# Performance work log

Measured on AMD Instinct MI355X. Metric: run time of the kernel, lower is better.

Reference implementation:

```python
import jax, jax.numpy as jnp
import numpy as np

CODEBOOK_SIZE = 8192
EMBED_DIM = 128
BETA = 0.25
TEMPERATURE = 0.1
EPS_NORM = 1e-12  # torch F.normalize eps


def _l2_normalize(x, axis=-1):
    n = jnp.linalg.norm(x, axis=axis, keepdims=True)
    return x / jnp.maximum(n, EPS_NORM)


def setup_inputs() -> dict:
    key = jax.random.key(0)
    kz, kw = jax.random.split(key)
    z = jax.random.normal(kz, (4, 4096, EMBED_DIM), dtype=jnp.float32)
    # torch init is uniform(-1/D, 1/D); normal also exercises the math fine,
    # but stay faithful to scale:
    W = jax.random.uniform(kw, (CODEBOOK_SIZE, EMBED_DIM), dtype=jnp.float32,
                           minval=-1.0 / EMBED_DIM, maxval=1.0 / EMBED_DIM)
    return {"z": z, "W": W}


def reference(z, W):
    orig_shape = z.shape
    z_flat = z.reshape(-1, EMBED_DIM)              # [N, D]
    N = z_flat.shape[0]

    z_norm = _l2_normalize(z_flat, axis=1)
    e_norm = _l2_normalize(W, axis=1)
    scores = z_norm @ e_norm.T                     # [N, K]

    idx = jnp.argmax(scores, axis=1)               # [N]
    z_q = W[idx].reshape(orig_shape)

    counts = jnp.zeros((CODEBOOK_SIZE,), jnp.float32).at[idx].add(1.0)
    e_mean = counts / N
    perplexity = jnp.exp(-jnp.sum(e_mean * jnp.log(e_mean + 1e-8)))

    sg = jax.lax.stop_gradient
    commit_loss = jnp.mean((sg(z_q) - z) ** 2) + BETA * jnp.mean((z_q - sg(z)) ** 2)

    z_q_st = z + sg(z_q - z)                        # straight-through

    log_probs = jax.nn.log_softmax(scores / TEMPERATURE, axis=1)  # [N, K]
    probs = jnp.exp(log_probs)
    P_avg = jnp.mean(probs, axis=0) + 1e-8
    entropy_loss = -jnp.sum(P_avg * jnp.log(P_avg))

    return (z_q_st, commit_loss, perplexity, entropy_loss)
```

## Files before the change

### kernel.cpp

```cpp
#include <hip/hip_runtime.h>
#include <hip/hip_bf16.h>
#include <math.h>

#define N_ROWS 16384
#define DIM 128
#define K_CODES 8192
#define SCALE_LOG2E 14.4269504088896341f
#define EPS2 0.0288539f
#define EPSF 1.00989e-3f

#define OFF_EN       0u
#define OFF_ZN       1048576u
#define OFF_EP       3145728u
#define OFF_ZP       4194304u
#define OFF_ZC       6291456u
#define OFF_PART     7340032u
#define OFF_PART2    7602176u
#define OFF_LINV     7864320u
#define OFF_IDX      7880704u
#define OFF_FLA      7897088u
#define OFF_FLB      7913472u
#define OFF_CNT      7929856u
#define OFF_P        7938048u
#define OFF_MSE      7946240u
#define OFF_NFA      7946241u
#define OFF_NFB      7946242u
#define OFF_REFBUF   7946244u
#define MEMSET_BYTES 196624u

typedef __bf16 bf16x8 __attribute__((ext_vector_type(8)));
typedef float  f32x4  __attribute__((ext_vector_type(4)));
#define MFMA16(a, b, c) __builtin_amdgcn_mfma_f32_16x16x32_bf16(a, b, c, 0, 0, 0)

#if defined(__has_builtin)
#if __has_builtin(__builtin_amdgcn_exp2f)
#define EXP2(x) __builtin_amdgcn_exp2f(x)
#endif
#endif
#ifndef EXP2
#define EXP2(x) __expf(0.69314718055994531f * (x))
#endif

__device__ __forceinline__ void gld_lds16(const ushort* g, ushort* l) {
    __builtin_amdgcn_global_load_lds(
        (const __attribute__((address_space(1))) unsigned int*)g,
        (__attribute__((address_space(3))) unsigned int*)l, 16, 0, 0);
}

__device__ __forceinline__ ushort f2bf(float x) {
    __hip_bfloat16 b = __float2bfloat16(x);
    return *reinterpret_cast<ushort*>(&b);
}
__device__ __forceinline__ float bf2f(ushort u) {
    __hip_bfloat16 b = *reinterpret_cast<__hip_bfloat16*>(&u);
    return __bfloat162float(b);
}

__device__ __forceinline__ void bf_store2(ushort* __restrict__ P, int T, int r,
                                          int rx, int k, ushort e0, ushort e1) {
    int g = k >> 6, kp = (k >> 3) & 7, j = k & 7;
    int off = (((((T << 2) + g) << 10) + (r << 3) + (kp ^ rx)) << 3) + j;
    *reinterpret_cast<ushort2*>(&P[off]) = make_ushort2(e0, e1);
}

__global__ __launch_bounds__(256) void k_prep(const float* __restrict__ z,
                                              const float* __restrict__ W,
                                              float* __restrict__ zN,
                                              float* __restrict__ eN,
                                              ushort* __restrict__ Zp,
                                              ushort* __restrict__ Ep) {
    int t = threadIdx.x, w = t >> 6, lane = t & 63;
    int row = blockIdx.x * 4 + w;
    const float* src; float* dstN; ushort* dstP; float sc;
    if (row < N_ROWS) { src = z; dstN = zN; dstP = Zp; sc = SCALE_LOG2E; }
    else { row -= N_ROWS; src = W; dstN = eN; dstP = Ep; sc = 1.0f; }
    float2 v = *reinterpret_cast<const float2*>(&src[(size_t)row * DIM + lane * 2]);
    float ss = v.x * v.x + v.y * v.y;
#pragma unroll
    for (int off = 32; off; off >>= 1) ss += __shfl_xor(ss, off);
    float nrm = fmaxf(sqrtf(ss), 1e-12f);
    float a = v.x / nrm, b = v.y / nrm;
    *reinterpret_cast<float2*>(&dstN[(size_t)row * DIM + lane * 2]) = make_float2(a, b);
    float as = a * sc, bs = b * sc;
    ushort ha = f2bf(as), hb = f2bf(bs);
    ushort la = f2bf(as - bf2f(ha)), lb = f2bf(bs - bf2f(hb));
    int T = row >> 7, r = row & 127, rx = r & 7, d = lane * 2;
    bf_store2(dstP, T, r, rx, d, ha, hb);
    bf_store2(dstP, T, r, rx, 128 + d, la, lb);
}

__global__ __launch_bounds__(256, 4) void k_p1(const ushort* __restrict__ Zp,
                                               const ushort* __restrict__ Ep,
                                               float4* __restrict__ part) {
    __shared__ ushort Bu[2][8192];
    int t = threadIdx.x, lane = t & 63, w = t >> 6;
    int rg = blockIdx.x >> 2, slice = blockIdx.x & 3;
    int wm = w >> 1, wn = w & 1;
    int n15 = lane & 15, quad = lane >> 4;
    int T = rg >> 1, rofs = (rg & 1) << 6;

    bf16x8 af[2][2][2];
#pragma unroll
    for (int ms = 0; ms < 2; ++ms) {
        int r = rofs + wm * 32 + ms * 16 + n15, rx = r & 7;
#pragma unroll
        for (int g = 0; g < 2; ++g)
#pragma unroll
            for (int kl = 0; kl < 2; ++kl)
                af[ms][g][kl] = *reinterpret_cast<const bf16x8*>(
                    &Zp[(((((T << 2) + g) << 10) + (r << 3) + (((kl * 4 + quad)) ^ rx)) << 3)]);
    }

    float sm[8], s2v[8], sl[8];
    unsigned si[8];
#pragma unroll
    for (int s = 0; s < 8; ++s) { sm[s] = -1e30f; s2v[s] = -1e30f; sl[s] = 0.f; si[s] = 0u; }

    {
        int Te = slice * 16, re = 0;
#pragma unroll
        for (int it = 0; it < 4; ++it) {
            int cpos = it * 256 + t;
            int g = cpos >> 9, loc = cpos & 511;
            gld_lds16(Ep + ((((Te << 2) + g) << 13) + (re << 6) + (loc << 3)),
                      &Bu[0][cpos << 3]);
        }
    }
    int bufc = 0;
    for (int ch = 0; ch < 32; ++ch) {
        __syncthreads();
        if (ch < 31) {
            int nx = ch + 1;
            int Te = slice * 16 + (nx >> 1), re = (nx & 1) << 6;
            ushort* dst = Bu[bufc ^ 1];
#pragma unroll
            for (int it = 0; it < 4; ++it) {
                int cpos = it * 256 + t;
                int g = cpos >> 9, loc = cpos & 511;
                gld_lds16(Ep + ((((Te << 2) + g) << 13) + (re << 6) + (loc << 3)),
                          &dst[cpos << 3]);
            }
        }
        const ushort* bsrc = Bu[bufc];
        f32x4 acc[2][2];
#pragma unroll
        for (int i = 0; i < 2; ++i)
#pragma unroll
            for (int j = 0; j < 2; ++j) acc[i][j] = (f32x4)2.0f;
#pragma unroll
        for (int g = 0; g < 2; ++g)
#pragma unroll
            for (int kl = 0; kl < 2; ++kl) {
                bf16x8 bfr[2];
#pragma unroll
                for (int ns = 0; ns < 2; ++ns) {
                    int c = wn * 32 + ns * 16 + n15;
                    int kx = (kl * 4 + quad) ^ (c & 7);
                    bfr[ns] = *reinterpret_cast<const bf16x8*>(
                        &bsrc[(((g << 9) + (c << 3) + kx) << 3)]);
                }
#pragma unroll
                for (int ms = 0; ms < 2; ++ms)
#pragma unroll
                    for (int ns = 0; ns < 2; ++ns)
                        acc[ms][ns] = MFMA16(af[ms][g][kl], bfr[ns], acc[ms][ns]);
            }
        unsigned cbase = (unsigned)(slice * 2048 + ch * 64 + wn * 32 + n15);
#pragma unroll
        for (int ms = 0; ms < 2; ++ms)
#pragma unroll
            for (int reg = 0; reg < 4; ++reg) {
                int s = ms * 4 + reg;
                float m = sm[s], m2 = s2v[s], l = sl[s];
                unsigned idx = si[s];
#pragma unroll
                for (int ns = 0; ns < 2; ++ns) {
                    float v = acc[ms][ns][reg];
                    l += EXP2(v);
                    m2 = __builtin_amdgcn_fmed3f(v, m, m2);
                    idx = (v > m) ? (cbase + ns * 16) : idx;
                    m = fmaxf(v, m);
                }
                sl[s] = l; sm[s] = m; s2v[s] = m2; si[s] = idx;
            }
        bufc ^= 1;
    }
#pragma unroll
    for (int ms = 0; ms < 2; ++ms)
#pragma unroll
        for (int reg = 0; reg < 4; ++reg) {
            int s = ms * 4 + reg;
            float m = sm[s], m2 = s2v[s], l = sl[s];
            unsigned idx = si[s];
#pragma unroll
            for (int off = 1; off < 16; off <<= 1) {
                float om  = __shfl_xor(m, off);
                float om2 = __shfl_xor(m2, off);
                float ol  = __shfl_xor(l, off);
                unsigned oi = (unsigned)__shfl_xor((int)idx, off);
                m2 = fmaxf(fmaxf(m2, om2), fminf(m, om));
                l += ol;
                bool take = (om > m) || (om == m && oi < idx);
                idx = take ? oi : idx;
                m = fmaxf(m, om);
            }
            if (n15 == 0) {
                int row = rg * 64 + wm * 32 + ms * 16 + quad * 4 + reg;
                part[slice * N_ROWS + row] = make_float4(m, l, __uint_as_float(idx), m2);
            }
        }
}

__global__ __launch_bounds__(256) void k_merge(const float4* __restrict__ part,
                                               float* __restrict__ linv_out,
                                               int* __restrict__ idx_out,
                                               unsigned int* __restrict__ counts,
                                               int* __restrict__ flaglistA,
                                               int* __restrict__ nfA) {
    int row = blockIdx.x * 256 + threadIdx.x;
    float m = -1e30f, m2 = -1e30f, l = 0.f;
    unsigned idx = 0u;
#pragma unroll
    for (int s = 0; s < 4; ++s) {
        float4 p = part[s * N_ROWS + row];
        float om = p.x, ol = p.y, om2 = p.w;
        unsigned oi = __float_as_uint(p.z);
        m2 = fmaxf(fmaxf(m2, om2), fminf(m, om));
        l += ol;
        bool take = (om > m) || (om == m && oi < idx);
        idx = take ? oi : idx;
        m = fmaxf(m, om);
    }
    linv_out[row] = 1.0f / l;
    idx_out[row] = (int)idx;
    atomicAdd(&counts[idx], 1u);
    if (m - m2 < EPS2) {
        int pos = atomicAdd(nfA, 1);
        if (pos < 8192) flaglistA[pos] = row;
    }
}

__global__ __launch_bounds__(256) void k_gather2(const ushort* __restrict__ Zp,
                                                 const int* __restrict__ flaglistA,
                                                 const int* __restrict__ nfA,
                                                 ushort* __restrict__ Zc) {
    int nf2 = *nfA; if (nf2 > 8192) nf2 = 8192;
    int total = nf2 * 32;
    const uint4* srcv = reinterpret_cast<const uint4*>(Zp);
    uint4* dstv = reinterpret_cast<uint4*>(Zc);
    for (int c = blockIdx.x * 256 + threadIdx.x; c < total; c += 65536) {
        int crow = c >> 5, g = (c >> 3) & 3, kp = c & 7;
        int row = flaglistA[crow];
        int Ts = row >> 7, rs = row & 127;
        int sidx = (((Ts << 2) + g) << 10) + (rs << 3) + (kp ^ (rs & 7));
        int Td = crow >> 6, rd = crow & 63;
        int didx = (((Td << 2) + g) << 9) + (rd << 3) + (kp ^ (rd & 7));
        dstv[didx] = srcv[sidx];
    }
}

__global__ __launch_bounds__(256, 2) void k_s2(const ushort* __restrict__ Zc,
                                               const ushort* __restrict__ Ep,
                                               const int* __restrict__ nfA,
                                               float4* __restrict__ part2) {
    __shared__ ushort Bu[2][8192];
    int nf2 = *nfA; if (nf2 > 8192) nf2 = 8192;
    int cg2 = blockIdx.x >> 3, csl = blockIdx.x & 7;
    if (cg2 * 64 >= nf2) return;
    int t = threadIdx.x, lane = t & 63, w = t >> 6;
    int wm = w >> 1, wn = w & 1;
    int n15 = lane & 15, quad = lane >> 4;

    bf16x8 af[2][4][2];
#pragma unroll
    for (int ms = 0; ms < 2; ++ms) {
        int r = wm * 32 + ms * 16 + n15, rx = r & 7;
#pragma unroll
        for (int gz = 0; gz < 4; ++gz)
#pragma unroll
            for (int kl = 0; kl < 2; ++kl)
                af[ms][gz][kl] = *reinterpret_cast<const bf16x8*>(
                    &Zc[(((((cg2 << 2) + gz) << 9) + (r << 3) + ((kl * 4 + quad) ^ rx)) << 3)]);
    }

    float sm[8], s2v[8];
    unsigned si[8];
#pragma unroll
    for (int s = 0; s < 8; ++s) { sm[s] = -1e30f; s2v[s] = -1e30f; si[s] = 0u; }

    {
        const ushort* gb = Ep + (((size_t)((csl * 8) << 2)) << 13);
#pragma unroll
        for (int it = 0; it < 4; ++it) {
            int cpos = it * 256 + t;
            gld_lds16(gb + (cpos << 3), &Bu[0][cpos << 3]);
        }
    }
    int bufc = 0;
    f32x4 acc[2][4];
#pragma unroll
    for (int i = 0; i < 2; ++i)
#pragma unroll
        for (int j = 0; j < 4; ++j) acc[i][j] = (f32x4)2.0f;

    for (int st = 0; st < 32; ++st) {
        __syncthreads();
        if (st < 31) {
            int nx = st + 1;
            const ushort* gb = Ep + (((size_t)(((csl * 8 + (nx >> 2)) << 2) + (nx & 3))) << 13);
            ushort* dst = Bu[bufc ^ 1];
#pragma unroll
            for (int it = 0; it < 4; ++it) {
                int cpos = it * 256 + t;
                gld_lds16(gb + (cpos << 3), &dst[cpos << 3]);
            }
        }
        const ushort* bsrc = Bu[bufc];
        int ge = st & 3;
        int a0 = ge & 1, a1 = (ge & 1) + 2;
        bool two = (ge < 2);
#pragma unroll
        for (int kl = 0; kl < 2; ++kl) {
            bf16x8 bfr[4];
#pragma unroll
            for (int ns = 0; ns < 4; ++ns) {
                int c = wn * 64 + ns * 16 + n15;
                int kx = (kl * 4 + quad) ^ (c & 7);
                bfr[ns] = *reinterpret_cast<const bf16x8*>(&bsrc[(((c << 3) + kx) << 3)]);
            }
#pragma unroll
            for (int ms = 0; ms < 2; ++ms)
#pragma unroll
                for (int ns = 0; ns < 4; ++ns)
                    acc[ms][ns] = MFMA16(af[ms][a0][kl], bfr[ns], acc[ms][ns]);
            if (two) {
#pragma unroll
                for (int ms = 0; ms < 2; ++ms)
#pragma unroll
                    for (int ns = 0; ns < 4; ++ns)
                        acc[ms][ns] = MFMA16(af[ms][a1][kl], bfr[ns], acc[ms][ns]);
            }
        }
        if (ge == 3) {
            int ch = st >> 2;
            unsigned cbase = (unsigned)((csl * 8 + ch) * 128 + wn * 64 + n15);
#pragma unroll
            for (int ms = 0; ms < 2; ++ms)
#pragma unroll
                for (int reg = 0; reg < 4; ++reg) {
                    int s = ms * 4 + reg;
                    float m = sm[s], m2 = s2v[s];
                    unsigned idx = si[s];
#pragma unroll
                    for (int ns = 0; ns < 4; ++ns) {
                        float v = acc[ms][ns][reg];
                        m2 = __builtin_amdgcn_fmed3f(v, m, m2);
                        idx = (v > m) ? (cbase + ns * 16) : idx;
                        m = fmaxf(v, m);
                    }
                    sm[s] = m; s2v[s] = m2; si[s] = idx;
                }
#pragma unroll
            for (int i = 0; i < 2; ++i)
#pragma unroll
                for (int j = 0; j < 4; ++j) acc[i][j] = (f32x4)2.0f;
        }
        bufc ^= 1;
    }
#pragma unroll
    for (int ms = 0; ms < 2; ++ms)
#pragma unroll
        for (int reg = 0; reg < 4; ++reg) {
            int s = ms * 4 + reg;
            float m = sm[s], m2 = s2v[s];
            unsigned idx = si[s];
#pragma unroll
            for (int off = 1; off < 16; off <<= 1) {
                float om  = __shfl_xor(m, off);
                float om2 = __shfl_xor(m2, off);
                unsigned oi = (unsigned)__shfl_xor((int)idx, off);
                m2 = fmaxf(fmaxf(m2, om2), fminf(m, om));
                bool take = (om > m) || (om == m && oi < idx);
                idx = take ? oi : idx;
                m = fmaxf(m, om);
            }
            if (n15 == 0) {
                int crow = cg2 * 64 + wm * 32 + ms * 16 + quad * 4 + reg;
                part2[csl * 8192 + crow] = make_float4(m, 0.f, __uint_as_float(idx), m2);
            }
        }
}

__global__ __launch_bounds__(256) void k_merge2(const float4* __restrict__ part2,
                                                const int* __restrict__ flaglistA,
                                                const int* __restrict__ nfA,
                                                int* __restrict__ idx_arr,
                                                unsigned int* __restrict__ counts,
                                                int* __restrict__ flaglistB,
                                                int* __restrict__ nfB) {
    int i = blockIdx.x * 256 + threadIdx.x;
    int nf2 = *nfA; if (nf2 > 8192) nf2 = 8192;
    if (i >= nf2) return;
    int row = flaglistA[i];
    float m = -1e30f, m2 = -1e30f;
    unsigned idx = 0u;
#pragma unroll
    for (int s = 0; s < 8; ++s) {
        float4 p = part2[s * 8192 + i];
        float om = p.x, om2 = p.w;
        unsigned oi = __float_as_uint(p.z);
        m2 = fmaxf(fmaxf(m2, om2), fminf(m, om));
        bool take = (om > m) || (om == m && oi < idx);
        idx = take ? oi : idx;
        m = fmaxf(m, om);
    }
    int newi = (int)idx, oldi = idx_arr[row];
    if (newi != oldi) {
        idx_arr[row] = newi;
        atomicAdd(&counts[oldi], 0xFFFFFFFFu);
        atomicAdd(&counts[newi], 1u);
    }
    if (m - m2 < EPSF) {
        int pos = atomicAdd(nfB, 1);
        if (pos < N_ROWS) flaglistB[pos] = row;
    }
}

__global__ __launch_bounds__(256) void k_refine(const float* __restrict__ zN,
                                                const float* __restrict__ eN,
                                                const int* __restrict__ flaglistB,
                                                const int* __restrict__ nfB,
                                                unsigned long long* __restrict__ refbuf) {
    int nf = *nfB;
    if (nf > N_ROWS) nf = N_ROWS;
    int csl = blockIdx.x & 7;
    int t = threadIdx.x;
    __shared__ float zl[DIM];
    for (int fi = blockIdx.x >> 3; fi < nf; fi += 512) {
        int row = flaglistB[fi];
        __syncthreads();
        if (t < DIM) zl[t] = zN[(size_t)row * DIM + t];
        __syncthreads();
        double best = -1e300;
        int bc = 0x7FFFFFFF;
#pragma unroll
        for (int j = 0; j < 4; ++j) {
            int c = csl * 1024 + j * 256 + t;
            const float* e = &eN[(size_t)c * DIM];
            double s = 0.0;
#pragma unroll 8
            for (int d = 0; d < DIM; ++d) s += (double)zl[d] * (double)e[d];
            if (s > best) { best = s; bc = c; }
        }
#pragma unroll
        for (int off = 1; off < 64; off <<= 1) {
            double ob = __shfl_xor(best, off);
            int oc = __shfl_xor(bc, off);
            if (ob > best || (ob == best && oc < bc)) { best = ob; bc = oc; }
        }
        if ((t & 63) == 0) {
            unsigned long long u = (unsigned long long)__double_as_longlong(best);
            u = (u & 0x8000000000000000ull) ? ~u : (u | 0x8000000000000000ull);
            unsigned long long key = (u & ~0x1FFFull) | (unsigned long long)(8191 - bc);
            atomicMax(&refbuf[row], key);
        }
    }
}

__global__ __launch_bounds__(256) void k_fixidx(const int* __restrict__ flaglistB,
                                                const int* __restrict__ nfB,
                                                const unsigned long long* __restrict__ refbuf,
                                                int* __restrict__ idx,
                                                unsigned int* __restrict__ counts) {
    int i = blockIdx.x * 256 + threadIdx.x;
    int nf = *nfB;
    if (nf > N_ROWS) nf = N_ROWS;
    if (i < nf) {
        int row = flaglistB[i];
        int newi = 8191 - (int)(refbuf[row] & 0x1FFFull);
        int oldi = idx[row];
        if (newi != oldi) {
            idx[row] = newi;
            atomicAdd(&counts[oldi], 0xFFFFFFFFu);
            atomicAdd(&counts[newi], 1u);
        }
    }
}

__global__ __launch_bounds__(256, 4) void k_p2(const ushort* __restrict__ Zp,
                                               const ushort* __restrict__ Ep,
                                               const float* __restrict__ linv_in,
                                               float* __restrict__ P_sum) {
    __shared__ ushort Bu[2][8192];
    int t = threadIdx.x, lane = t & 63, w = t >> 6;
    int cg = blockIdx.x >> 2, rslice = blockIdx.x & 3;
    int wm = w >> 1, wn = w & 1;
    int n15 = lane & 15, quad = lane >> 4;
    int T = cg >> 1, cofs = (cg & 1) << 6;

    bf16x8 af[2][2][2];
#pragma unroll
    for (int ms = 0; ms < 2; ++ms) {
        int c = cofs + wm * 32 + ms * 16 + n15, cx = c & 7;
#pragma unroll
        for (int g = 0; g < 2; ++g)
#pragma unroll
            for (int kl = 0; kl < 2; ++kl)
                af[ms][g][kl] = *reinterpret_cast<const bf16x8*>(
                    &Ep[(((((T << 2) + g) << 10) + (c << 3) + ((kl * 4 + quad) ^ cx)) << 3)]);
    }

    float pacc[8];
#pragma unroll
    for (int s = 0; s < 8; ++s) pacc[s] = 0.f;

    {
        int Tz = rslice * 32, re = 0;
#pragma unroll
        for (int it = 0; it < 4; ++it) {
            int cpos = it * 256 + t;
            int g = cpos >> 9, loc = cpos & 511;
            gld_lds16(Zp + ((((Tz << 2) + g) << 13) + (re << 6) + (loc << 3)),
                      &Bu[0][cpos << 3]);
        }
    }
    int bufc = 0;
    for (int ch = 0; ch < 64; ++ch) {
        __syncthreads();
        if (ch < 63) {
            int nx = ch + 1;
            int Tz = rslice * 32 + (nx >> 1), re = (nx & 1) << 6;
            ushort* dst = Bu[bufc ^ 1];
#pragma unroll
            for (int it = 0; it < 4; ++it) {
                int cpos = it * 256 + t;
                int g = cpos >> 9, loc = cpos & 511;
                gld_lds16(Zp + ((((Tz << 2) + g) << 13) + (re << 6) + (loc << 3)),
                          &dst[cpos << 3]);
            }
        }
        const ushort* bsrc = Bu[bufc];
        f32x4 acc[2][2];
#pragma unroll
        for (int i = 0; i < 2; ++i)
#pragma unroll
            for (int j = 0; j < 2; ++j) acc[i][j] = (f32x4)2.0f;
#pragma unroll
        for (int g = 0; g < 2; ++g)
#pragma unroll
            for (int kl = 0; kl < 2; ++kl) {
                bf16x8 bfr[2];
#pragma unroll
                for (int ns = 0; ns < 2; ++ns) {
                    int r = wn * 32 + ns * 16 + n15;
                    int kx = (kl * 4 + quad) ^ (r & 7);
                    bfr[ns] = *reinterpret_cast<const bf16x8*>(
                        &bsrc[(((g << 9) + (r << 3) + kx) << 3)]);
                }
#pragma unroll
                for (int ms = 0; ms < 2; ++ms)
#pragma unroll
                    for (int ns = 0; ns < 2; ++ns)
                        acc[ms][ns] = MFMA16(af[ms][g][kl], bfr[ns], acc[ms][ns]);
            }
        int rbase = rslice * 4096 + ch * 64 + wn * 32 + n15;
        float li[2];
#pragma unroll
        for (int ns = 0; ns < 2; ++ns) li[ns] = linv_in[rbase + ns * 16];
#pragma unroll
        for (int ms = 0; ms < 2; ++ms)
#pragma unroll
            for (int reg = 0; reg < 4; ++reg) {
                int s = ms * 4 + reg;
                float p = pacc[s];
#pragma unroll
                for (int ns = 0; ns < 2; ++ns)
                    p = fmaf(EXP2(acc[ms][ns][reg]), li[ns], p);
                pacc[s] = p;
            }
        bufc ^= 1;
    }
#pragma unroll
    for (int s = 0; s < 8; ++s) {
#pragma unroll
        for (int off = 1; off < 16; off <<= 1) pacc[s] += __shfl_xor(pacc[s], off);
    }
    if (n15 == 0) {
#pragma unroll
        for (int ms = 0; ms < 2; ++ms)
#pragma unroll
            for (int reg = 0; reg < 4; ++reg)
                atomicAdd(&P_sum[cg * 64 + wm * 32 + ms * 16 + quad * 4 + reg],
                          pacc[ms * 4 + reg]);
    }
}

__global__ __launch_bounds__(256) void k_gather(const float* __restrict__ z,
                                                const float* __restrict__ W,
                                                const int* __restrict__ idx,
                                                float* __restrict__ out,
                                                float* __restrict__ mse) {
    int v = blockIdx.x * 256 + threadIdx.x;
    int row = v >> 5;
    int id = idx[row];
    float4 q = *reinterpret_cast<const float4*>(&W[(size_t)id * DIM + (v & 31) * 4]);
    float4 zz = *reinterpret_cast<const float4*>(&z[(size_t)v * 4]);
    float dx = q.x - zz.x, dy = q.y - zz.y, dz = q.z - zz.z, dw = q.w - zz.w;
    *reinterpret_cast<float4*>(&out[(size_t)v * 4]) = q;
    float e = dx * dx + dy * dy + dz * dz + dw * dw;
#pragma unroll
    for (int off = 1; off < 64; off <<= 1) e += __shfl_xor(e, off);
    __shared__ float red[4];
    int lane = threadIdx.x & 63, wv = threadIdx.x >> 6;
    if (lane == 0) red[wv] = e;
    __syncthreads();
    if (threadIdx.x == 0) atomicAdd(mse, red[0] + red[1] + red[2] + red[3]);
}

__global__ __launch_bounds__(256) void k_finalize(const unsigned int* __restrict__ counts,
                                                  const float* __restrict__ P_sum,
                                                  const float* __restrict__ mse,
                                                  float* __restrict__ out) {
    int t = threadIdx.x;
    float s1 = 0.f, s2 = 0.f;
    for (int k = t; k < K_CODES; k += 256) {
        float em = (float)counts[k] * (1.0f / 16384.0f);
        s1 += em * logf(em + 1e-8f);
        float p = P_sum[k] * (1.0f / 16384.0f) + 1e-8f;
        s2 += p * logf(p);
    }
#pragma unroll
    for (int off = 1; off < 64; off <<= 1) {
        s1 += __shfl_xor(s1, off);
        s2 += __shfl_xor(s2, off);
    }
    __shared__ float r1[4], r2[4];
    int lane = t & 63, wv = t >> 6;
    if (lane == 0) { r1[wv] = s1; r2[wv] = s2; }
    __syncthreads();
    if (t == 0) {
        float S1 = r1[0] + r1[1] + r1[2] + r1[3];
        float S2 = r2[0] + r2[1] + r2[2] + r2[3];
        out[2097152] = 1.25f * mse[0] * (1.0f / 2097152.0f);
        out[2097153] = expf(-S1);
        out[2097154] = -S2;
    }
}

extern "C" void kernel_launch(void* const* d_in, const int* in_sizes, int n_in,
                              void* d_out, int out_size, void* d_ws, size_t ws_size,
                              hipStream_t stream) {
    (void)in_sizes; (void)n_in; (void)out_size; (void)ws_size;
    const float* z = (const float*)d_in[0];
    const float* W = (const float*)d_in[1];
    float* ws = (float*)d_ws;
    float* eN = ws + OFF_EN;
    float* zN = ws + OFF_ZN;
    ushort* Ep = (ushort*)(ws + OFF_EP);
    ushort* Zp = (ushort*)(ws + OFF_ZP);
    ushort* Zc = (ushort*)(ws + OFF_ZC);
    float4* part = (float4*)(ws + OFF_PART);
    float4* part2 = (float4*)(ws + OFF_PART2);
    float* linv = ws + OFF_LINV;
    int* idx = (int*)(ws + OFF_IDX);
    int* flaglistA = (int*)(ws + OFF_FLA);
    int* flaglistB = (int*)(ws + OFF_FLB);
    unsigned int* counts = (unsigned int*)(ws + OFF_CNT);
    float* P = ws + OFF_P;
    float* mse = ws + OFF_MSE;
    int* nfA = (int*)(ws + OFF_NFA);
    int* nfB = (int*)(ws + OFF_NFB);
    unsigned long long* refbuf = (unsigned long long*)(ws + OFF_REFBUF);
    float* out = (float*)d_out;

    hipMemsetAsync(ws + OFF_CNT, 0, MEMSET_BYTES, stream);
    k_prep<<<(N_ROWS + K_CODES) / 4, 256, 0, stream>>>(z, W, zN, eN, Zp, Ep);
    k_p1<<<1024, 256, 0, stream>>>(Zp, Ep, part);
    k_merge<<<N_ROWS / 256, 256, 0, stream>>>(part, linv, idx, counts, flaglistA, nfA);
    k_gather2<<<256, 256, 0, stream>>>(Zp, flaglistA, nfA, Zc);
    k_s2<<<1024, 256, 0, stream>>>(Zc, Ep, nfA, part2);
    k_merge2<<<32, 256, 0, stream>>>(part2, flaglistA, nfA, idx, counts, flaglistB, nfB);
    k_refine<<<4096, 256, 0, stream>>>(zN, eN, flaglistB, nfB, refbuf);
    k_fixidx<<<64, 256, 0, stream>>>(flaglistB, nfB, refbuf, idx, counts);
    k_p2<<<512, 256, 0, stream>>>(Zp, Ep, linv, P);
    k_gather<<<(N_ROWS * DIM / 4) / 256, 256, 0, stream>>>(z, W, idx, out, mse);
    k_finalize<<<1, 256, 0, stream>>>(counts, P, mse, out);
}
```

Measured before the change: 299.0 us.

## Drop intermediate bf16 rescoring stage and spread MSE atomics across slots

Removes the gather2/s2/merge2 second-pass bf16 rescoring of ambiguous rows, so every row flagged by the first merge goes straight to the fp32 exact refine kernel. This cuts three kernel launches and a partial GEMM. In exchange, refine may process more rows, since the flag list is no longer narrowed by the tighter EPSF threshold. The MSE reduction now writes to 256 padded partial slots instead of a single atomic, and finalize reduces those slots.

```diff
diff --git a/kernel.cpp b/kernel.cpp
--- a/kernel.cpp
+++ b/kernel.cpp
@@ -7,26 +7,23 @@
 #define K_CODES 8192
 #define SCALE_LOG2E 14.4269504088896341f
 #define EPS2 0.0288539f
-#define EPSF 1.00989e-3f
 
 #define OFF_EN       0u
 #define OFF_ZN       1048576u
 #define OFF_EP       3145728u
 #define OFF_ZP       4194304u
-#define OFF_ZC       6291456u
 #define OFF_PART     7340032u
-#define OFF_PART2    7602176u
 #define OFF_LINV     7864320u
 #define OFF_IDX      7880704u
 #define OFF_FLA      7897088u
-#define OFF_FLB      7913472u
 #define OFF_CNT      7929856u
 #define OFF_P        7938048u
 #define OFF_MSE      7946240u
 #define OFF_NFA      7946241u
 #define OFF_NFB      7946242u
 #define OFF_REFBUF   7946244u
-#define MEMSET_BYTES 196624u
+#define OFF_MSEP     7979012u
+#define MEMSET_BYTES 213008u
 
 typedef __bf16 bf16x8 __attribute__((ext_vector_type(8)));
 typedef float  f32x4  __attribute__((ext_vector_type(4)));
@@ -240,204 +237,18 @@
     }
 }
 
-__global__ __launch_bounds__(256) void k_gather2(const ushort* __restrict__ Zp,
-                                                 const int* __restrict__ flaglistA,
-                                                 const int* __restrict__ nfA,
-                                                 ushort* __restrict__ Zc) {
-    int nf2 = *nfA; if (nf2 > 8192) nf2 = 8192;
-    int total = nf2 * 32;
-    const uint4* srcv = reinterpret_cast<const uint4*>(Zp);
-    uint4* dstv = reinterpret_cast<uint4*>(Zc);
-    for (int c = blockIdx.x * 256 + threadIdx.x; c < total; c += 65536) {
-        int crow = c >> 5, g = (c >> 3) & 3, kp = c & 7;
-        int row = flaglistA[crow];
-        int Ts = row >> 7, rs = row & 127;
-        int sidx = (((Ts << 2) + g) << 10) + (rs << 3) + (kp ^ (rs & 7));
-        int Td = crow >> 6, rd = crow & 63;
-        int didx = (((Td << 2) + g) << 9) + (rd << 3) + (kp ^ (rd & 7));
-        dstv[didx] = srcv[sidx];
-    }
-}
-
-__global__ __launch_bounds__(256, 2) void k_s2(const ushort* __restrict__ Zc,
-                                               const ushort* __restrict__ Ep,
-                                               const int* __restrict__ nfA,
-                                               float4* __restrict__ part2) {
-    __shared__ ushort Bu[2][8192];
-    int nf2 = *nfA; if (nf2 > 8192) nf2 = 8192;
-    int cg2 = blockIdx.x >> 3, csl = blockIdx.x & 7;
-    if (cg2 * 64 >= nf2) return;
-    int t = threadIdx.x, lane = t & 63, w = t >> 6;
-    int wm = w >> 1, wn = w & 1;
-    int n15 = lane & 15, quad = lane >> 4;
-
-    bf16x8 af[2][4][2];
-#pragma unroll
-    for (int ms = 0; ms < 2; ++ms) {
-        int r = wm * 32 + ms * 16 + n15, rx = r & 7;
-#pragma unroll
-        for (int gz = 0; gz < 4; ++gz)
-#pragma unroll
-            for (int kl = 0; kl < 2; ++kl)
-                af[ms][gz][kl] = *reinterpret_cast<const bf16x8*>(
-                    &Zc[(((((cg2 << 2) + gz) << 9) + (r << 3) + ((kl * 4 + quad) ^ rx)) << 3)]);
-    }
-
-    float sm[8], s2v[8];
-    unsigned si[8];
-#pragma unroll
-    for (int s = 0; s < 8; ++s) { sm[s] = -1e30f; s2v[s] = -1e30f; si[s] = 0u; }
-
-    {
-        const ushort* gb = Ep + (((size_t)((csl * 8) << 2)) << 13);
-#pragma unroll
-        for (int it = 0; it < 4; ++it) {
-            int cpos = it * 256 + t;
-            gld_lds16(gb + (cpos << 3), &Bu[0][cpos << 3]);
-        }
-    }
-    int bufc = 0;
-    f32x4 acc[2][4];
-#pragma unroll
-    for (int i = 0; i < 2; ++i)
-#pragma unroll
-        for (int j = 0; j < 4; ++j) acc[i][j] = (f32x4)2.0f;
-
-    for (int st = 0; st < 32; ++st) {
-        __syncthreads();
-        if (st < 31) {
-            int nx = st + 1;
-            const ushort* gb = Ep + (((size_t)(((csl * 8 + (nx >> 2)) << 2) + (nx & 3))) << 13);
-            ushort* dst = Bu[bufc ^ 1];
-#pragma unroll
-            for (int it = 0; it < 4; ++it) {
-                int cpos = it * 256 + t;
-                gld_lds16(gb + (cpos << 3), &dst[cpos << 3]);
-            }
-        }
-        const ushort* bsrc = Bu[bufc];
-        int ge = st & 3;
-        int a0 = ge & 1, a1 = (ge & 1) + 2;
-        bool two = (ge < 2);
-#pragma unroll
-        for (int kl = 0; kl < 2; ++kl) {
-            bf16x8 bfr[4];
-#pragma unroll
-            for (int ns = 0; ns < 4; ++ns) {
-                int c = wn * 64 + ns * 16 + n15;
-                int kx = (kl * 4 + quad) ^ (c & 7);
-                bfr[ns] = *reinterpret_cast<const bf16x8*>(&bsrc[(((c << 3) + kx) << 3)]);
-            }
-#pragma unroll
-            for (int ms = 0; ms < 2; ++ms)
-#pragma unroll
-                for (int ns = 0; ns < 4; ++ns)
-                    acc[ms][ns] = MFMA16(af[ms][a0][kl], bfr[ns], acc[ms][ns]);
-            if (two) {
-#pragma unroll
-                for (int ms = 0; ms < 2; ++ms)
-#pragma unroll
-                    for (int ns = 0; ns < 4; ++ns)
-                        acc[ms][ns] = MFMA16(af[ms][a1][kl], bfr[ns], acc[ms][ns]);
-            }
-        }
-        if (ge == 3) {
-            int ch = st >> 2;
-            unsigned cbase = (unsigned)((csl * 8 + ch) * 128 + wn * 64 + n15);
-#pragma unroll
-            for (int ms = 0; ms < 2; ++ms)
-#pragma unroll
-                for (int reg = 0; reg < 4; ++reg) {
-                    int s = ms * 4 + reg;
-                    float m = sm[s], m2 = s2v[s];
-                    unsigned idx = si[s];
-#pragma unroll
-                    for (int ns = 0; ns < 4; ++ns) {
-                        float v = acc[ms][ns][reg];
-                        m2 = __builtin_amdgcn_fmed3f(v, m, m2);
-                        idx = (v > m) ? (cbase + ns * 16) : idx;
-                        m = fmaxf(v, m);
-                    }
-                    sm[s] = m; s2v[s] = m2; si[s] = idx;
-                }
-#pragma unroll
-            for (int i = 0; i < 2; ++i)
-#pragma unroll
-                for (int j = 0; j < 4; ++j) acc[i][j] = (f32x4)2.0f;
-        }
-        bufc ^= 1;
-    }
-#pragma unroll
-    for (int ms = 0; ms < 2; ++ms)
-#pragma unroll
-        for (int reg = 0; reg < 4; ++reg) {
-            int s = ms * 4 + reg;
-            float m = sm[s], m2 = s2v[s];
-            unsigned idx = si[s];
-#pragma unroll
-            for (int off = 1; off < 16; off <<= 1) {
-                float om  = __shfl_xor(m, off);
-                float om2 = __shfl_xor(m2, off);
-                unsigned oi = (unsigned)__shfl_xor((int)idx, off);
-                m2 = fmaxf(fmaxf(m2, om2), fminf(m, om));
-                bool take = (om > m) || (om == m && oi < idx);
-                idx = take ? oi : idx;
-                m = fmaxf(m, om);
-            }
-            if (n15 == 0) {
-                int crow = cg2 * 64 + wm * 32 + ms * 16 + quad * 4 + reg;
-                part2[csl * 8192 + crow] = make_float4(m, 0.f, __uint_as_float(idx), m2);
-            }
-        }
-}
-
-__global__ __launch_bounds__(256) void k_merge2(const float4* __restrict__ part2,
-                                                const int* __restrict__ flaglistA,
-                                                const int* __restrict__ nfA,
-                                                int* __restrict__ idx_arr,
-                                                unsigned int* __restrict__ counts,
-                                                int* __restrict__ flaglistB,
-                                                int* __restrict__ nfB) {
-    int i = blockIdx.x * 256 + threadIdx.x;
-    int nf2 = *nfA; if (nf2 > 8192) nf2 = 8192;
-    if (i >= nf2) return;
-    int row = flaglistA[i];
-    float m = -1e30f, m2 = -1e30f;
-    unsigned idx = 0u;
-#pragma unroll
-    for (int s = 0; s < 8; ++s) {
-        float4 p = part2[s * 8192 + i];
-        float om = p.x, om2 = p.w;
-        unsigned oi = __float_as_uint(p.z);
-        m2 = fmaxf(fmaxf(m2, om2), fminf(m, om));
-        bool take = (om > m) || (om == m && oi < idx);
-        idx = take ? oi : idx;
-        m = fmaxf(m, om);
-    }
-    int newi = (int)idx, oldi = idx_arr[row];
-    if (newi != oldi) {
-        idx_arr[row] = newi;
-        atomicAdd(&counts[oldi], 0xFFFFFFFFu);
-        atomicAdd(&counts[newi], 1u);
-    }
-    if (m - m2 < EPSF) {
-        int pos = atomicAdd(nfB, 1);
-        if (pos < N_ROWS) flaglistB[pos] = row;
-    }
-}
-
 __global__ __launch_bounds__(256) void k_refine(const float* __restrict__ zN,
                                                 const float* __restrict__ eN,
-                                                const int* __restrict__ flaglistB,
-                                                const int* __restrict__ nfB,
+                                                const int* __restrict__ flaglist,
+                                                const int* __restrict__ nfp,
                                                 unsigned long long* __restrict__ refbuf) {
-    int nf = *nfB;
-    if (nf > N_ROWS) nf = N_ROWS;
+    int nf = *nfp;
+    if (nf > 8192) nf = 8192;
     int csl = blockIdx.x & 7;
     int t = threadIdx.x;
     __shared__ float zl[DIM];
     for (int fi = blockIdx.x >> 3; fi < nf; fi += 512) {
-        int row = flaglistB[fi];
+        int row = flaglist[fi];
         __syncthreads();
         if (t < DIM) zl[t] = zN[(size_t)row * DIM + t];
         __syncthreads();
@@ -467,16 +278,16 @@
     }
 }
 
-__global__ __launch_bounds__(256) void k_fixidx(const int* __restrict__ flaglistB,
-                                                const int* __restrict__ nfB,
+__global__ __launch_bounds__(256) void k_fixidx(const int* __restrict__ flaglist,
+                                                const int* __restrict__ nfp,
                                                 const unsigned long long* __restrict__ refbuf,
                                                 int* __restrict__ idx,
                                                 unsigned int* __restrict__ counts) {
     int i = blockIdx.x * 256 + threadIdx.x;
-    int nf = *nfB;
-    if (nf > N_ROWS) nf = N_ROWS;
+    int nf = *nfp;
+    if (nf > 8192) nf = 8192;
     if (i < nf) {
-        int row = flaglistB[i];
+        int row = flaglist[i];
         int newi = 8191 - (int)(refbuf[row] & 0x1FFFull);
         int oldi = idx[row];
         if (newi != oldi) {
@@ -599,7 +410,7 @@
                                                 const float* __restrict__ W,
                                                 const int* __restrict__ idx,
                                                 float* __restrict__ out,
-                                                float* __restrict__ mse) {
+                                                float* __restrict__ msep) {
     int v = blockIdx.x * 256 + threadIdx.x;
     int row = v >> 5;
     int id = idx[row];
@@ -614,15 +425,17 @@
     int lane = threadIdx.x & 63, wv = threadIdx.x >> 6;
     if (lane == 0) red[wv] = e;
     __syncthreads();
-    if (threadIdx.x == 0) atomicAdd(mse, red[0] + red[1] + red[2] + red[3]);
+    if (threadIdx.x == 0)
+        atomicAdd(&msep[(blockIdx.x & 255) * 16], red[0] + red[1] + red[2] + red[3]);
 }
 
 __global__ __launch_bounds__(256) void k_finalize(const unsigned int* __restrict__ counts,
                                                   const float* __restrict__ P_sum,
-                                                  const float* __restrict__ mse,
+                                                  const float* __restrict__ msep,
                                                   float* __restrict__ out) {
     int t = threadIdx.x;
     float s1 = 0.f, s2 = 0.f;
+    float s3 = msep[t * 16];
     for (int k = t; k < K_CODES; k += 256) {
         float em = (float)counts[k] * (1.0f / 16384.0f);
         s1 += em * logf(em + 1e-8f);
@@ -633,15 +446,17 @@
     for (int off = 1; off < 64; off <<= 1) {
         s1 += __shfl_xor(s1, off);
         s2 += __shfl_xor(s2, off);
-    }
-    __shared__ float r1[4], r2[4];
+        s3 += __shfl_xor(s3, off);
+    }
+    __shared__ float r1[4], r2[4], r3[4];
     int lane = t & 63, wv = t >> 6;
-    if (lane == 0) { r1[wv] = s1; r2[wv] = s2; }
+    if (lane == 0) { r1[wv] = s1; r2[wv] = s2; r3[wv] = s3; }
     __syncthreads();
     if (t == 0) {
         float S1 = r1[0] + r1[1] + r1[2] + r1[3];
         float S2 = r2[0] + r2[1] + r2[2] + r2[3];
-        out[2097152] = 1.25f * mse[0] * (1.0f / 2097152.0f);
+        float S3 = r3[0] + r3[1] + r3[2] + r3[3];
+        out[2097152] = 1.25f * S3 * (1.0f / 2097152.0f);
         out[2097153] = expf(-S1);
         out[2097154] = -S2;
     }
@@ -658,31 +473,24 @@
     float* zN = ws + OFF_ZN;
     ushort* Ep = (ushort*)(ws + OFF_EP);
     ushort* Zp = (ushort*)(ws + OFF_ZP);
-    ushort* Zc = (ushort*)(ws + OFF_ZC);
     float4* part = (float4*)(ws + OFF_PART);
-    float4* part2 = (float4*)(ws + OFF_PART2);
     float* linv = ws + OFF_LINV;
     int* idx = (int*)(ws + OFF_IDX);
     int* flaglistA = (int*)(ws + OFF_FLA);
-    int* flaglistB = (int*)(ws + OFF_FLB);
     unsigned int* counts = (unsigned int*)(ws + OFF_CNT);
     float* P = ws + OFF_P;
-    float* mse = ws + OFF_MSE;
     int* nfA = (int*)(ws + OFF_NFA);
-    int* nfB = (int*)(ws + OFF_NFB);
     unsigned long long* refbuf = (unsigned long long*)(ws + OFF_REFBUF);
+    float* msep = ws + OFF_MSEP;
     float* out = (float*)d_out;
 
     hipMemsetAsync(ws + OFF_CNT, 0, MEMSET_BYTES, stream);
     k_prep<<<(N_ROWS + K_CODES) / 4, 256, 0, stream>>>(z, W, zN, eN, Zp, Ep);
     k_p1<<<1024, 256, 0, stream>>>(Zp, Ep, part);
     k_merge<<<N_ROWS / 256, 256, 0, stream>>>(part, linv, idx, counts, flaglistA, nfA);
-    k_gather2<<<256, 256, 0, stream>>>(Zp, flaglistA, nfA, Zc);
-    k_s2<<<1024, 256, 0, stream>>>(Zc, Ep, nfA, part2);
-    k_merge2<<<32, 256, 0, stream>>>(part2, flaglistA, nfA, idx, counts, flaglistB, nfB);
-    k_refine<<<4096, 256, 0, stream>>>(zN, eN, flaglistB, nfB, refbuf);
-    k_fixidx<<<64, 256, 0, stream>>>(flaglistB, nfB, refbuf, idx, counts);
+    k_refine<<<4096, 256, 0, stream>>>(zN, eN, flaglistA, nfA, refbuf);
+    k_fixidx<<<64, 256, 0, stream>>>(flaglistA, nfA, refbuf, idx, counts);
     k_p2<<<512, 256, 0, stream>>>(Zp, Ep, linv, P);
-    k_gather<<<(N_ROWS * DIM / 4) / 256, 256, 0, stream>>>(z, W, idx, out, mse);
-    k_finalize<<<1, 256, 0, stream>>>(counts, P, mse, out);
-}
+    k_gather<<<(N_ROWS * DIM / 4) / 256, 256, 0, stream>>>(z, W, idx, out, msep);
+    k_finalize<<<1, 256, 0, stream>>>(counts, P, msep, out);
+}
```

Measured after the change: 874.5 us. +192.5%, slower.

## Fuse flagged-row gather into stage-2 scoring, spread MSE atomics, drain loads before barriers

Applied to the files above, without the earlier changes.

Removes the separate k_gather2 kernel. The stage-2 kernel now indexes the packed Z tile directly through the flag list, and the flag-list capacity rises to all rows, with grids sized to match. This saves one launch and a compacting copy, at the cost of scattered A-fragment loads. The MSE reduction in k_gather now writes to 256 padded partial slots instead of one contended atomic, and k_finalize sums them. Explicit vmcnt(0) waits are also added before the double-buffer barriers, which fixes LDS async-load visibility but may reduce overlap.

```diff
diff --git a/kernel.cpp b/kernel.cpp
--- a/kernel.cpp
+++ b/kernel.cpp
@@ -9,24 +9,26 @@
 #define EPS2 0.0288539f
 #define EPSF 1.00989e-3f
 
+#define VM_DRAIN() asm volatile("s_waitcnt vmcnt(0)" ::: "memory")
+
 #define OFF_EN       0u
 #define OFF_ZN       1048576u
 #define OFF_EP       3145728u
 #define OFF_ZP       4194304u
-#define OFF_ZC       6291456u
-#define OFF_PART     7340032u
-#define OFF_PART2    7602176u
-#define OFF_LINV     7864320u
-#define OFF_IDX      7880704u
-#define OFF_FLA      7897088u
-#define OFF_FLB      7913472u
-#define OFF_CNT      7929856u
-#define OFF_P        7938048u
-#define OFF_MSE      7946240u
-#define OFF_NFA      7946241u
-#define OFF_NFB      7946242u
-#define OFF_REFBUF   7946244u
-#define MEMSET_BYTES 196624u
+#define OFF_PART     6291456u
+#define OFF_PART2    6553600u
+#define OFF_LINV     7077888u
+#define OFF_IDX      7094272u
+#define OFF_FLA      7110656u
+#define OFF_FLB      7127040u
+#define OFF_CNT      7143424u
+#define OFF_P        7151616u
+#define OFF_MSE      7159808u
+#define OFF_NFA      7159809u
+#define OFF_NFB      7159810u
+#define OFF_REFBUF   7159812u
+#define OFF_MSEP     7192580u
+#define MEMSET_BYTES 213008u
 
 typedef __bf16 bf16x8 __attribute__((ext_vector_type(8)));
 typedef float  f32x4  __attribute__((ext_vector_type(4)));
@@ -128,6 +130,7 @@
     }
     int bufc = 0;
     for (int ch = 0; ch < 32; ++ch) {
+        VM_DRAIN();
         __syncthreads();
         if (ch < 31) {
             int nx = ch + 1;
@@ -236,35 +239,17 @@
     atomicAdd(&counts[idx], 1u);
     if (m - m2 < EPS2) {
         int pos = atomicAdd(nfA, 1);
-        if (pos < 8192) flaglistA[pos] = row;
-    }
-}
-
-__global__ __launch_bounds__(256) void k_gather2(const ushort* __restrict__ Zp,
-                                                 const int* __restrict__ flaglistA,
-                                                 const int* __restrict__ nfA,
-                                                 ushort* __restrict__ Zc) {
-    int nf2 = *nfA; if (nf2 > 8192) nf2 = 8192;
-    int total = nf2 * 32;
-    const uint4* srcv = reinterpret_cast<const uint4*>(Zp);
-    uint4* dstv = reinterpret_cast<uint4*>(Zc);
-    for (int c = blockIdx.x * 256 + threadIdx.x; c < total; c += 65536) {
-        int crow = c >> 5, g = (c >> 3) & 3, kp = c & 7;
-        int row = flaglistA[crow];
-        int Ts = row >> 7, rs = row & 127;
-        int sidx = (((Ts << 2) + g) << 10) + (rs << 3) + (kp ^ (rs & 7));
-        int Td = crow >> 6, rd = crow & 63;
-        int didx = (((Td << 2) + g) << 9) + (rd << 3) + (kp ^ (rd & 7));
-        dstv[didx] = srcv[sidx];
-    }
-}
-
-__global__ __launch_bounds__(256, 2) void k_s2(const ushort* __restrict__ Zc,
+        if (pos < N_ROWS) flaglistA[pos] = row;
+    }
+}
+
+__global__ __launch_bounds__(256, 2) void k_s2(const ushort* __restrict__ Zp,
                                                const ushort* __restrict__ Ep,
+                                               const int* __restrict__ flaglistA,
                                                const int* __restrict__ nfA,
                                                float4* __restrict__ part2) {
     __shared__ ushort Bu[2][8192];
-    int nf2 = *nfA; if (nf2 > 8192) nf2 = 8192;
+    int nf2 = *nfA; if (nf2 > N_ROWS) nf2 = N_ROWS;
     int cg2 = blockIdx.x >> 3, csl = blockIdx.x & 7;
     if (cg2 * 64 >= nf2) return;
     int t = threadIdx.x, lane = t & 63, w = t >> 6;
@@ -274,13 +259,15 @@
     bf16x8 af[2][4][2];
 #pragma unroll
     for (int ms = 0; ms < 2; ++ms) {
-        int r = wm * 32 + ms * 16 + n15, rx = r & 7;
+        int crow = cg2 * 64 + wm * 32 + ms * 16 + n15;
+        int row = flaglistA[crow < nf2 ? crow : 0] & (N_ROWS - 1);
+        int T = row >> 7, rs = row & 127, rx = rs & 7;
 #pragma unroll
         for (int gz = 0; gz < 4; ++gz)
 #pragma unroll
             for (int kl = 0; kl < 2; ++kl)
                 af[ms][gz][kl] = *reinterpret_cast<const bf16x8*>(
-                    &Zc[(((((cg2 << 2) + gz) << 9) + (r << 3) + ((kl * 4 + quad) ^ rx)) << 3)]);
+                    &Zp[(((((T << 2) + gz) << 10) + (rs << 3) + ((kl * 4 + quad) ^ rx)) << 3)]);
     }
 
     float sm[8], s2v[8];
@@ -304,6 +291,7 @@
         for (int j = 0; j < 4; ++j) acc[i][j] = (f32x4)2.0f;
 
     for (int st = 0; st < 32; ++st) {
+        VM_DRAIN();
         __syncthreads();
         if (st < 31) {
             int nx = st + 1;
@@ -386,7 +374,7 @@
             }
             if (n15 == 0) {
                 int crow = cg2 * 64 + wm * 32 + ms * 16 + quad * 4 + reg;
-                part2[csl * 8192 + crow] = make_float4(m, 0.f, __uint_as_float(idx), m2);
+                part2[csl * N_ROWS + crow] = make_float4(m, 0.f, __uint_as_float(idx), m2);
             }
         }
 }
@@ -399,14 +387,14 @@
                                                 int* __restrict__ flaglistB,
                                                 int* __restrict__ nfB) {
     int i = blockIdx.x * 256 + threadIdx.x;
-    int nf2 = *nfA; if (nf2 > 8192) nf2 = 8192;
+    int nf2 = *nfA; if (nf2 > N_ROWS) nf2 = N_ROWS;
     if (i >= nf2) return;
     int row = flaglistA[i];
     float m = -1e30f, m2 = -1e30f;
     unsigned idx = 0u;
 #pragma unroll
     for (int s = 0; s < 8; ++s) {
-        float4 p = part2[s * 8192 + i];
+        float4 p = part2[s * N_ROWS + i];
         float om = p.x, om2 = p.w;
         unsigned oi = __float_as_uint(p.z);
         m2 = fmaxf(fmaxf(m2, om2), fminf(m, om));
@@ -526,6 +514,7 @@
     }
     int bufc = 0;
     for (int ch = 0; ch < 64; ++ch) {
+        VM_DRAIN();
         __syncthreads();
         if (ch < 63) {
             int nx = ch + 1;
@@ -599,7 +588,7 @@
                                                 const float* __restrict__ W,
                                                 const int* __restrict__ idx,
                                                 float* __restrict__ out,
-                                                float* __restrict__ mse) {
+                                                float* __restrict__ msep) {
     int v = blockIdx.x * 256 + threadIdx.x;
     int row = v >> 5;
     int id = idx[row];
@@ -614,15 +603,17 @@
     int lane = threadIdx.x & 63, wv = threadIdx.x >> 6;
     if (lane == 0) red[wv] = e;
     __syncthreads();
-    if (threadIdx.x == 0) atomicAdd(mse, red[0] + red[1] + red[2] + red[3]);
+    if (threadIdx.x == 0)
+        atomicAdd(&msep[(blockIdx.x & 255) * 16], red[0] + red[1] + red[2] + red[3]);
 }
 
 __global__ __launch_bounds__(256) void k_finalize(const unsigned int* __restrict__ counts,
                                                   const float* __restrict__ P_sum,
-                                                  const float* __restrict__ mse,
+                                                  const float* __restrict__ msep,
                                                   float* __restrict__ out) {
     int t = threadIdx.x;
     float s1 = 0.f, s2 = 0.f;
+    float s3 = msep[t * 16];
     for (int k = t; k < K_CODES; k += 256) {
         float em = (float)counts[k] * (1.0f / 16384.0f);
         s1 += em * logf(em + 1e-8f);
@@ -633,15 +624,17 @@
     for (int off = 1; off < 64; off <<= 1) {
         s1 += __shfl_xor(s1, off);
         s2 += __shfl_xor(s2, off);
-    }
-    __shared__ float r1[4], r2[4];
+        s3 += __shfl_xor(s3, off);
+    }
+    __shared__ float r1[4], r2[4], r3[4];
     int lane = t & 63, wv = t >> 6;
-    if (lane == 0) { r1[wv] = s1; r2[wv] = s2; }
+    if (lane == 0) { r1[wv] = s1; r2[wv] = s2; r3[wv] = s3; }
     __syncthreads();
     if (t == 0) {
         float S1 = r1[0] + r1[1] + r1[2] + r1[3];
         float S2 = r2[0] + r2[1] + r2[2] + r2[3];
-        out[2097152] = 1.25f * mse[0] * (1.0f / 2097152.0f);
+        float S3 = r3[0] + r3[1] + r3[2] + r3[3];
+        out[2097152] = 1.25f * S3 * (1.0f / 2097152.0f);
         out[2097153] = expf(-S1);
         out[2097154] = -S2;
     }
@@ -658,7 +651,6 @@
     float* zN = ws + OFF_ZN;
     ushort* Ep = (ushort*)(ws + OFF_EP);
     ushort* Zp = (ushort*)(ws + OFF_ZP);
-    ushort* Zc = (ushort*)(ws + OFF_ZC);
     float4* part = (float4*)(ws + OFF_PART);
     float4* part2 = (float4*)(ws + OFF_PART2);
     float* linv = ws + OFF_LINV;
@@ -667,22 +659,21 @@
     int* flaglistB = (int*)(ws + OFF_FLB);
     unsigned int* counts = (unsigned int*)(ws + OFF_CNT);
     float* P = ws + OFF_P;
-    float* mse = ws + OFF_MSE;
     int* nfA = (int*)(ws + OFF_NFA);
     int* nfB = (int*)(ws + OFF_NFB);
     unsigned long long* refbuf = (unsigned long long*)(ws + OFF_REFBUF);
+    float* msep = ws + OFF_MSEP;
     float* out = (float*)d_out;
 
     hipMemsetAsync(ws + OFF_CNT, 0, MEMSET_BYTES, stream);
     k_prep<<<(N_ROWS + K_CODES) / 4, 256, 0, stream>>>(z, W, zN, eN, Zp, Ep);
     k_p1<<<1024, 256, 0, stream>>>(Zp, Ep, part);
     k_merge<<<N_ROWS / 256, 256, 0, stream>>>(part, linv, idx, counts, flaglistA, nfA);
-    k_gather2<<<256, 256, 0, stream>>>(Zp, flaglistA, nfA, Zc);
-    k_s2<<<1024, 256, 0, stream>>>(Zc, Ep, nfA, part2);
-    k_merge2<<<32, 256, 0, stream>>>(part2, flaglistA, nfA, idx, counts, flaglistB, nfB);
+    k_s2<<<2048, 256, 0, stream>>>(Zp, Ep, flaglistA, nfA, part2);
+    k_merge2<<<64, 256, 0, stream>>>(part2, flaglistA, nfA, idx, counts, flaglistB, nfB);
     k_refine<<<4096, 256, 0, stream>>>(zN, eN, flaglistB, nfB, refbuf);
     k_fixidx<<<64, 256, 0, stream>>>(flaglistB, nfB, refbuf, idx, counts);
     k_p2<<<512, 256, 0, stream>>>(Zp, Ep, linv, P);
-    k_gather<<<(N_ROWS * DIM / 4) / 256, 256, 0, stream>>>(z, W, idx, out, mse);
-    k_finalize<<<1, 256, 0, stream>>>(counts, P, mse, out);
-}
+    k_gather<<<(N_ROWS * DIM / 4) / 256, 256, 0, stream>>>(z, W, idx, out, msep);
+    k_finalize<<<1, 256, 0, stream>>>(counts, P, msep, out);
+}
```

Measured after the change: 269.3 us. 1.11x faster.
